# Kernel tuning notes

Measured on AMD Instinct MI355X. Metric: run time of the kernel, lower is better.

Reference implementation:

```python
import jax, jax.numpy as jnp
import numpy as np

B, L, D_MODEL, D_STATE, D_CONV, EXPAND = 2, 1024, 1024, 16, 4, 2
D_INNER = D_MODEL * EXPAND


def setup_inputs() -> dict:
    key = jax.random.key(0)
    ks = jax.random.split(key, 8)
    s = lambda fan: 1.0 / np.sqrt(fan)
    x = jax.random.normal(ks[0], (B, L, D_MODEL), jnp.float32)
    in_proj_w = jax.random.normal(ks[1], (D_MODEL, 2 * D_INNER), jnp.float32) * s(D_MODEL)
    conv_w = jax.random.normal(ks[2], (D_INNER, 1, D_CONV), jnp.float32) * s(D_CONV)
    conv_b = jax.random.normal(ks[3], (D_INNER,), jnp.float32) * 0.01
    x_proj_w = jax.random.normal(ks[4], (D_INNER, 2 * D_STATE + D_INNER), jnp.float32) * s(D_INNER)
    dt_proj_w = jax.random.normal(ks[5], (D_INNER, D_INNER), jnp.float32) * s(D_INNER)
    dt_proj_b = jax.random.normal(ks[6], (D_INNER,), jnp.float32) * 0.01
    A_log = jnp.log(jnp.tile(jnp.arange(1, D_STATE + 1, dtype=jnp.float32)[None, :], (D_INNER, 1)))
    D = jnp.ones((D_INNER,), jnp.float32)
    out_proj_w = jax.random.normal(ks[7], (D_INNER, D_MODEL), jnp.float32) * s(D_INNER)
    return {"x": x, "in_proj_w": in_proj_w, "conv_w": conv_w, "conv_b": conv_b,
            "x_proj_w": x_proj_w, "dt_proj_w": dt_proj_w, "dt_proj_b": dt_proj_b,
            "A_log": A_log, "D": D, "out_proj_w": out_proj_w}


def _mamba_forward(x, in_proj_w, conv_w, conv_b, x_proj_w, dt_proj_w, dt_proj_b, A_log, D, out_proj_w):
    Bb, Ll, _ = x.shape
    d_inner, _, d_conv = conv_w.shape
    d_state = A_log.shape[1]
    # input projection and gate split
    xz = x @ in_proj_w                       # [B, L, 2*Di]
    x_inner, z = jnp.split(xz, 2, axis=-1)   # each [B, L, Di]
    # causal depthwise conv (left pad k-1, truncate to L == torch pad+slice)
    xc = jnp.transpose(x_inner, (0, 2, 1))   # [B, Di, L]
    xc = jax.lax.conv_general_dilated(
        xc, conv_w, window_strides=(1,), padding=[(d_conv - 1, 0)],
        dimension_numbers=("NCH", "OIH", "NCH"), feature_group_count=d_inner)
    xc = xc + conv_b[None, :, None]
    u = jax.nn.silu(jnp.transpose(xc, (0, 2, 1)))  # [B, L, Di]
    # SSM parameter projections
    ssm = u @ x_proj_w                        # [B, L, 2N+Di]
    B_ssm = ssm[..., :d_state]                # [B, L, N]
    C_ssm = ssm[..., d_state:2 * d_state]     # [B, L, N]
    dt = jax.nn.softplus(ssm[..., 2 * d_state:] @ dt_proj_w + dt_proj_b)  # [B, L, Di]
    A_real = -jnp.exp(A_log)                  # [Di, N]
    # selective scan over sequence (recurrence via lax.scan)
    def step(h, inp):
        dt_t, B_t, u_t = inp                  # [B,Di], [B,N], [B,Di]
        dA = jnp.exp(dt_t[..., None] * A_real)            # [B, Di, N]
        dBu = dt_t[..., None] * B_t[:, None, :] * u_t[..., None]
        h = dA * h + dBu
        return h, h
    h0 = jnp.zeros((Bb, d_inner, d_state), x.dtype)
    xs = (jnp.swapaxes(dt, 0, 1), jnp.swapaxes(B_ssm, 0, 1), jnp.swapaxes(u, 0, 1))
    _, states = jax.lax.scan(step, h0, xs)    # [L, B, Di, N]
    y = jnp.einsum("lbdn,lbn->lbd", states, jnp.swapaxes(C_ssm, 0, 1))
    y = jnp.swapaxes(y, 0, 1) + D * u         # skip connection
    y = y * jax.nn.silu(z)                    # gating
    return y @ out_proj_w                     # [B, L, d_model]


def reference(x, in_proj_w, conv_w, conv_b, x_proj_w, dt_proj_w, dt_proj_b, A_log, D, out_proj_w):
    return _mamba_forward(x, in_proj_w, conv_w, conv_b, x_proj_w, dt_proj_w, dt_proj_b, A_log, D, out_proj_w)
```

## Files before the change

kernel.cpp:

```cpp
#include <hip/hip_runtime.h>
#include <hip/hip_bf16.h>

#define BB 2
#define LL 1024
#define DMODEL 1024
#define DINNER 2048
#define DSTATE 16
#define DCONV 4
#define MM (BB * LL)
#define N_XZ 4096
#define N_SSM 2080
#define N_SSM_PAD 2176
#define CCH 32
#define LCH 32

typedef __hip_bfloat16 bf16;
typedef short bf16x8 __attribute__((ext_vector_type(8)));
typedef float f32x4 __attribute__((ext_vector_type(4)));

__device__ __forceinline__ void load16_lds(const bf16* g, bf16* l) {
    __builtin_amdgcn_global_load_lds(
        (const __attribute__((address_space(1))) void*)g,
        (__attribute__((address_space(3))) void*)l,
        16, 0, 0);
}

__global__ void cvt_kernel(const float* __restrict__ in, bf16* __restrict__ out, int n) {
    int i = blockIdx.x * blockDim.x + threadIdx.x;
    if (i < n) out[i] = __float2bfloat16(in[i]);
}

__global__ void transpose_cvt_kernel(const float* __restrict__ in, bf16* __restrict__ out,
                                     int K, int N) {
    __shared__ float tile[32][33];
    const int nb = blockIdx.x * 32, kb = blockIdx.y * 32;
    const int tx = threadIdx.x & 31;
    const int ty = threadIdx.x >> 5;
    #pragma unroll
    for (int i = 0; i < 32; i += 8) {
        int k = kb + ty + i, n = nb + tx;
        tile[ty + i][tx] = (k < K && n < N) ? in[(size_t)k * N + n] : 0.f;
    }
    __syncthreads();
    #pragma unroll
    for (int i = 0; i < 32; i += 8) {
        int n = nb + ty + i, k = kb + tx;
        if (n < N && k < K) out[(size_t)n * K + k] = __float2bfloat16(tile[tx][ty + i]);
    }
}

#define TM 128
#define TN 64
#define TK 32
template<int EPI, int KSPLIT = 1>
__global__ __launch_bounds__(256) void mfma_gemm(
    const bf16* __restrict__ A, int lda,
    const bf16* __restrict__ Wt, int ldw,
    float* __restrict__ Cf, bf16* __restrict__ Cb, int ldc,
    const float* __restrict__ bias,
    int N, int K)
{
    __shared__ __align__(16) bf16 As[TM * TK];
    __shared__ __align__(16) bf16 Bs[TN * TK];
    const int tid = threadIdx.x;
    const int wave = tid >> 6, lane = tid & 63;
    const int wm = (wave >> 1) * 64, wn = (wave & 1) * 32;
    const int m0 = blockIdx.y * TM, n0 = blockIdx.x * TN;
    const int lm = lane & 15, kq = lane >> 4;

    const int srow = lane >> 2;
    const int cg = ((lane & 3) - ((srow >> 1) & 3)) & 3;
    const bf16* gA0 = A + (size_t)(m0 + wave * 16 + srow) * lda + cg * 8;
    const bf16* gA1 = A + (size_t)(m0 + wave * 16 + 64 + srow) * lda + cg * 8;
    const bf16* gB  = Wt + (size_t)(n0 + wave * 16 + srow) * ldw + cg * 8;
    bf16* As0 = &As[(wave * 16) * TK];
    bf16* As1 = &As[(wave * 16 + 64) * TK];
    bf16* Bs0 = &Bs[(wave * 16) * TK];

    const int soff = ((kq + ((lm >> 1) & 3)) & 3) * 8;

    const int Kc = K / KSPLIT;
    const int kbeg = (KSPLIT > 1) ? blockIdx.z * Kc : 0;

    f32x4 acc[4][2] = {};

    for (int it = 0; it < Kc; it += TK) {
        const int k0 = kbeg + it;
        load16_lds(gA0 + k0, As0);
        load16_lds(gA1 + k0, As1);
        load16_lds(gB + k0, Bs0);
        __syncthreads();

        bf16x8 af[4], bfr[2];
        #pragma unroll
        for (int i = 0; i < 4; ++i)
            af[i] = *(const bf16x8*)(&As[(wm + i * 16 + lm) * TK + soff]);
        #pragma unroll
        for (int j = 0; j < 2; ++j)
            bfr[j] = *(const bf16x8*)(&Bs[(wn + j * 16 + lm) * TK + soff]);
        #pragma unroll
        for (int i = 0; i < 4; ++i)
            #pragma unroll
            for (int j = 0; j < 2; ++j)
                acc[i][j] = __builtin_amdgcn_mfma_f32_16x16x32_bf16(af[i], bfr[j], acc[i][j], 0, 0, 0);
        __syncthreads();
    }

    #pragma unroll
    for (int i = 0; i < 4; ++i) {
        #pragma unroll
        for (int j = 0; j < 2; ++j) {
            int gcol = n0 + wn + j * 16 + lm;
            if ((EPI == 0 || EPI == 3) && gcol >= N) continue;
            #pragma unroll
            for (int r = 0; r < 4; ++r) {
                int grow = m0 + wm + i * 16 + kq * 4 + r;
                float v = acc[i][j][r];
                if (EPI == 1) {
                    v += bias[gcol];
                    v = (v > 20.f) ? v : log1pf(__expf(v));
                    Cf[(size_t)grow * ldc + gcol] = v;
                } else if (EPI == 2) {
                    if (KSPLIT > 1) atomicAdd(&Cf[(size_t)grow * ldc + gcol], v);
                    else            Cf[(size_t)grow * ldc + gcol] = v;
                } else if (EPI == 3) {
                    if (gcol < 32) Cf[(size_t)grow * 32 + gcol] = v;
                    else           Cb[(size_t)grow * ldc + gcol] = __float2bfloat16(v);
                } else {
                    Cb[(size_t)grow * ldc + gcol] = __float2bfloat16(v);
                }
            }
        }
    }
}

__global__ void conv_silu_kernel(const bf16* __restrict__ xz,
                                 const float* __restrict__ conv_w,
                                 const float* __restrict__ conv_b,
                                 bf16* __restrict__ u)
{
    int idx = blockIdx.x * blockDim.x + threadIdx.x;
    if (idx >= BB * LL * DINNER) return;
    int d = idx & (DINNER - 1);
    int l = (idx >> 11) & (LL - 1);
    int b = idx >> 21;
    float acc = conv_b[d];
    #pragma unroll
    for (int j = 0; j < DCONV; ++j) {
        int ll = l - (DCONV - 1) + j;
        if (ll >= 0) {
            float xv = (float)xz[((size_t)(b * LL + ll)) * N_XZ + d];
            acc = fmaf(conv_w[d * DCONV + j], xv, acc);
        }
    }
    u[idx] = __float2bfloat16(acc / (1.f + __expf(-acc)));
}

__global__ __launch_bounds__(256) void scan_phase_a(
    const float* __restrict__ dt, const bf16* __restrict__ u,
    const float* __restrict__ BC,
    const float* __restrict__ A_log,
    float* __restrict__ chunkP, float* __restrict__ chunkH)
{
    const int d = blockIdx.x * 256 + threadIdx.x;
    const int c = blockIdx.y, b = blockIdx.z;
    const int l0 = c * LCH;

    float A[DSTATE];
    {
        const f32x4* ap = (const f32x4*)(A_log + d * DSTATE);
        #pragma unroll
        for (int q = 0; q < 4; ++q) {
            f32x4 v = ap[q];
            #pragma unroll
            for (int r = 0; r < 4; ++r) A[q * 4 + r] = -__expf(v[r]);
        }
    }
    float h[DSTATE];
    #pragma unroll
    for (int n = 0; n < DSTATE; ++n) h[n] = 0.f;
    float sdt = 0.f;

    const float* dtp = dt + ((size_t)b * LL + l0) * DINNER + d;
    const bf16* up = u + ((size_t)b * LL + l0) * DINNER + d;
    const float* bcp = BC + ((size_t)b * LL + l0) * 32;

    #pragma unroll 2
    for (int i = 0; i < LCH; ++i) {
        float dtv = *dtp;
        float uv  = (float)*up;
        float du  = dtv * uv;
        f32x4 Bv[4];
        #pragma unroll
        for (int q = 0; q < 4; ++q) Bv[q] = *(const f32x4*)(bcp + q * 4);
        #pragma unroll
        for (int n = 0; n < DSTATE; ++n) {
            float a = __expf(dtv * A[n]);
            h[n] = fmaf(a, h[n], du * Bv[n >> 2][n & 3]);
        }
        sdt += dtv;
        dtp += DINNER; up += DINNER; bcp += 32;
    }

    size_t idx = (((size_t)b * CCH + c) * DINNER + d) * DSTATE;
    #pragma unroll
    for (int q = 0; q < 4; ++q) {
        f32x4 pv, hv;
        #pragma unroll
        for (int r = 0; r < 4; ++r) { pv[r] = __expf(A[q * 4 + r] * sdt); hv[r] = h[q * 4 + r]; }
        *(f32x4*)(chunkP + idx + q * 4) = pv;
        *(f32x4*)(chunkH + idx + q * 4) = hv;
    }
}

__global__ __launch_bounds__(256) void scan_phase_p(
    const float* __restrict__ chunkP, float* __restrict__ chunkH)
{
    int gid = blockIdx.x * 256 + threadIdx.x;
    int n = gid & 15;
    int d = (gid >> 4) & (DINNER - 1);
    int b = gid >> 15;
    const size_t stride = (size_t)DINNER * DSTATE;
    size_t idx = ((size_t)b * CCH * DINNER + d) * DSTATE + n;
    float H = 0.f;
    for (int c = 0; c < CCH; ++c) {
        float P  = chunkP[idx];
        float hl = chunkH[idx];
        chunkH[idx] = H;
        H = fmaf(P, H, hl);
        idx += stride;
    }
}

__global__ __launch_bounds__(256) void scan_phase_b(
    const float* __restrict__ dt, bf16* __restrict__ u,
    const float* __restrict__ BC, const bf16* __restrict__ xz,
    const float* __restrict__ A_log, const float* __restrict__ Dp,
    const float* __restrict__ chunkH)
{
    const int d = blockIdx.x * 256 + threadIdx.x;
    const int c = blockIdx.y, b = blockIdx.z;
    const int l0 = c * LCH;

    float A[DSTATE];
    {
        const f32x4* ap = (const f32x4*)(A_log + d * DSTATE);
        #pragma unroll
        for (int q = 0; q < 4; ++q) {
            f32x4 v = ap[q];
            #pragma unroll
            for (int r = 0; r < 4; ++r) A[q * 4 + r] = -__expf(v[r]);
        }
    }
    const float Dd = Dp[d];
    float h[DSTATE];
    {
        size_t idx = (((size_t)b * CCH + c) * DINNER + d) * DSTATE;
        #pragma unroll
        for (int q = 0; q < 4; ++q) {
            f32x4 v = *(const f32x4*)(chunkH + idx + q * 4);
            #pragma unroll
            for (int r = 0; r < 4; ++r) h[q * 4 + r] = v[r];
        }
    }

    const float* dtp = dt + ((size_t)b * LL + l0) * DINNER + d;
    bf16* up = u + ((size_t)b * LL + l0) * DINNER + d;
    const float* bcp = BC + ((size_t)b * LL + l0) * 32;
    const bf16* zp = xz + ((size_t)b * LL + l0) * N_XZ + DINNER + d;

    #pragma unroll 2
    for (int i = 0; i < LCH; ++i) {
        float dtv = *dtp;
        float uv  = (float)*up;
        float du  = dtv * uv;
        f32x4 Bv[4], Cv[4];
        #pragma unroll
        for (int q = 0; q < 4; ++q) {
            Bv[q] = *(const f32x4*)(bcp + q * 4);
            Cv[q] = *(const f32x4*)(bcp + 16 + q * 4);
        }
        float acc = 0.f;
        #pragma unroll
        for (int n = 0; n < DSTATE; ++n) {
            float a = __expf(dtv * A[n]);
            h[n] = fmaf(a, h[n], du * Bv[n >> 2][n & 3]);
            acc = fmaf(h[n], Cv[n >> 2][n & 3], acc);
        }
        float zv = (float)*zp;
        acc = fmaf(Dd, uv, acc);
        acc *= zv / (1.f + __expf(-zv));
        *up = __float2bfloat16(acc);
        dtp += DINNER; up += DINNER; bcp += 32; zp += N_XZ;
    }
}

extern "C" void kernel_launch(void* const* d_in, const int* in_sizes, int n_in,
                              void* d_out, int out_size, void* d_ws, size_t ws_size,
                              hipStream_t stream) {
    const float* x         = (const float*)d_in[0];
    const float* in_proj_w = (const float*)d_in[1];
    const float* conv_w    = (const float*)d_in[2];
    const float* conv_b    = (const float*)d_in[3];
    const float* x_proj_w  = (const float*)d_in[4];
    const float* dt_proj_w = (const float*)d_in[5];
    const float* dt_proj_b = (const float*)d_in[6];
    const float* A_log     = (const float*)d_in[7];
    const float* Dp        = (const float*)d_in[8];
    const float* out_proj_w= (const float*)d_in[9];
    float* out = (float*)d_out;

    char* p = (char*)d_ws;
    float* dt   = (float*)p;                          p += (size_t)MM * DINNER * 4;
    bf16*  xbf  = (bf16*)dt;
    bf16*  xz   = (bf16*)p;                           p += (size_t)MM * N_XZ * 2;
    bf16*  u    = (bf16*)p;                           p += (size_t)MM * DINNER * 2;
    bf16*  ssm  = (bf16*)p;                           p += (size_t)MM * N_SSM * 2;
    bf16*  Wt1  = (bf16*)p;                           p += (size_t)N_XZ * DMODEL * 2;
    bf16*  Wt2  = (bf16*)p;                           p += (size_t)N_SSM_PAD * DINNER * 2;
    bf16*  Wt3  = (bf16*)p;                           p += (size_t)DINNER * DINNER * 2;
    bf16*  Wt4  = (bf16*)p;                           p += (size_t)DMODEL * DINNER * 2;
    float* BC   = (float*)p;                          p += (size_t)MM * 32 * 4;
    float* chunkP = (float*)Wt1;
    float* chunkH = (float*)Wt2;

    {
        int n = MM * DMODEL;
        cvt_kernel<<<(n + 255) / 256, 256, 0, stream>>>(x, xbf, n);
        transpose_cvt_kernel<<<dim3(N_XZ / 32, DMODEL / 32), 256, 0, stream>>>(in_proj_w, Wt1, DMODEL, N_XZ);
        transpose_cvt_kernel<<<dim3((N_SSM + 31) / 32, DINNER / 32), 256, 0, stream>>>(x_proj_w, Wt2, DINNER, N_SSM);
        transpose_cvt_kernel<<<dim3(DINNER / 32, DINNER / 32), 256, 0, stream>>>(dt_proj_w, Wt3, DINNER, DINNER);
        transpose_cvt_kernel<<<dim3(DMODEL / 32, DINNER / 32), 256, 0, stream>>>(out_proj_w, Wt4, DINNER, DMODEL);
    }
    mfma_gemm<0><<<dim3(N_XZ / TN, MM / TM), 256, 0, stream>>>(
        xbf, DMODEL, Wt1, DMODEL, nullptr, xz, N_XZ, nullptr, N_XZ, DMODEL);
    {
        int n = BB * LL * DINNER;
        conv_silu_kernel<<<(n + 255) / 256, 256, 0, stream>>>(xz, conv_w, conv_b, u);
    }
    mfma_gemm<3><<<dim3(N_SSM_PAD / TN, MM / TM), 256, 0, stream>>>(
        u, DINNER, Wt2, DINNER, BC, ssm, N_SSM, nullptr, N_SSM, DINNER);
    mfma_gemm<1><<<dim3(DINNER / TN, MM / TM), 256, 0, stream>>>(
        ssm + 2 * DSTATE, N_SSM, Wt3, DINNER, dt, nullptr, DINNER, dt_proj_b, DINNER, DINNER);
    scan_phase_a<<<dim3(DINNER / 256, CCH, BB), 256, 0, stream>>>(dt, u, BC, A_log, chunkP, chunkH);
    scan_phase_p<<<dim3(BB * DINNER * DSTATE / 256), 256, 0, stream>>>(chunkP, chunkH);
    scan_phase_b<<<dim3(DINNER / 256, CCH, BB), 256, 0, stream>>>(dt, u, BC, xz, A_log, Dp, chunkH);
    hipMemsetAsync(out, 0, (size_t)out_size * sizeof(float), stream);
    mfma_gemm<2, 2><<<dim3(DMODEL / TN, MM / TM, 2), 256, 0, stream>>>(
        u, DINNER, Wt4, DINNER, out, nullptr, DMODEL, nullptr, DMODEL, DINNER);
}
```

Before: 374.7 us.

## Fuse weight/input conversion launches and double GEMM K-tile with XOR swizzle

Merges the five float-to-bf16 conversion and transpose launches into a single prep kernel that dispatches on block index. It also vectorizes the x conversion with float4 loads. The GEMM K-tile grows from 32 to 64, with a new XOR-swizzled LDS layout and two MFMA k-steps per barrier pair, so the loop synchronizes half as often. The cost is larger LDS tiles and more fragment registers per thread, which may lower occupancy.

```diff
diff --git a/kernel.cpp b/kernel.cpp
--- a/kernel.cpp
+++ b/kernel.cpp
@@ -25,33 +25,48 @@
         16, 0, 0);
 }
 
-__global__ void cvt_kernel(const float* __restrict__ in, bf16* __restrict__ out, int n) {
-    int i = blockIdx.x * blockDim.x + threadIdx.x;
-    if (i < n) out[i] = __float2bfloat16(in[i]);
-}
-
-__global__ void transpose_cvt_kernel(const float* __restrict__ in, bf16* __restrict__ out,
-                                     int K, int N) {
+__global__ __launch_bounds__(256) void prep_kernel(
+    const float* __restrict__ x, bf16* __restrict__ xbf,
+    const float* __restrict__ w1, bf16* __restrict__ o1,
+    const float* __restrict__ w2, bf16* __restrict__ o2,
+    const float* __restrict__ w3, bf16* __restrict__ o3,
+    const float* __restrict__ w4, bf16* __restrict__ o4)
+{
+    int bid = blockIdx.x;
+    const float* src; bf16* dst; int K, N, tn, tk;
+    if (bid < 4096)        { src = w1; dst = o1; K = 1024; N = 4096; tn = bid & 127; tk = bid >> 7; }
+    else if (bid < 8256)   { bid -= 4096;  src = w2; dst = o2; K = 2048; N = 2080; tn = bid % 65; tk = bid / 65; }
+    else if (bid < 12352)  { bid -= 8256;  src = w3; dst = o3; K = 2048; N = 2048; tn = bid & 63; tk = bid >> 6; }
+    else if (bid < 14400)  { bid -= 12352; src = w4; dst = o4; K = 2048; N = 1024; tn = bid & 31; tk = bid >> 5; }
+    else {
+        bid -= 14400;
+        int i = (bid * 256 + threadIdx.x) * 4;
+        float4 v = *(const float4*)(x + i);
+        xbf[i + 0] = __float2bfloat16(v.x);
+        xbf[i + 1] = __float2bfloat16(v.y);
+        xbf[i + 2] = __float2bfloat16(v.z);
+        xbf[i + 3] = __float2bfloat16(v.w);
+        return;
+    }
     __shared__ float tile[32][33];
-    const int nb = blockIdx.x * 32, kb = blockIdx.y * 32;
-    const int tx = threadIdx.x & 31;
-    const int ty = threadIdx.x >> 5;
+    const int nb = tn * 32, kb = tk * 32;
+    const int tx = threadIdx.x & 31, ty = threadIdx.x >> 5;
     #pragma unroll
     for (int i = 0; i < 32; i += 8) {
         int k = kb + ty + i, n = nb + tx;
-        tile[ty + i][tx] = (k < K && n < N) ? in[(size_t)k * N + n] : 0.f;
+        tile[ty + i][tx] = (k < K && n < N) ? src[(size_t)k * N + n] : 0.f;
     }
     __syncthreads();
     #pragma unroll
     for (int i = 0; i < 32; i += 8) {
         int n = nb + ty + i, k = kb + tx;
-        if (n < N && k < K) out[(size_t)n * K + k] = __float2bfloat16(tile[tx][ty + i]);
+        if (n < N && k < K) dst[(size_t)n * K + k] = __float2bfloat16(tile[tx][ty + i]);
     }
 }
 
 #define TM 128
 #define TN 64
-#define TK 32
+#define TK 64
 template<int EPI, int KSPLIT = 1>
 __global__ __launch_bounds__(256) void mfma_gemm(
     const bf16* __restrict__ A, int lda,
@@ -68,41 +83,47 @@
     const int m0 = blockIdx.y * TM, n0 = blockIdx.x * TN;
     const int lm = lane & 15, kq = lane >> 4;
 
-    const int srow = lane >> 2;
-    const int cg = ((lane & 3) - ((srow >> 1) & 3)) & 3;
-    const bf16* gA0 = A + (size_t)(m0 + wave * 16 + srow) * lda + cg * 8;
-    const bf16* gA1 = A + (size_t)(m0 + wave * 16 + 64 + srow) * lda + cg * 8;
-    const bf16* gB  = Wt + (size_t)(n0 + wave * 16 + srow) * ldw + cg * 8;
-    bf16* As0 = &As[(wave * 16) * TK];
-    bf16* As1 = &As[(wave * 16 + 64) * TK];
-    bf16* Bs0 = &Bs[(wave * 16) * TK];
-
-    const int soff = ((kq + ((lm >> 1) & 3)) & 3) * 8;
+    const int srow = lane >> 3;
+    const int schunk = (lane & 7) ^ srow;
+    const bf16* gA = A + (size_t)(m0 + wave * 32 + srow) * lda + schunk * 8;
+    const bf16* gB = Wt + (size_t)(n0 + wave * 16 + srow) * ldw + schunk * 8;
+    bf16* lA = &As[(wave * 32) * TK];
+    bf16* lB = &Bs[(wave * 16) * TK];
 
     const int Kc = K / KSPLIT;
     const int kbeg = (KSPLIT > 1) ? blockIdx.z * Kc : 0;
 
     f32x4 acc[4][2] = {};
+    const int fsw = (lm & 7);
 
     for (int it = 0; it < Kc; it += TK) {
         const int k0 = kbeg + it;
-        load16_lds(gA0 + k0, As0);
-        load16_lds(gA1 + k0, As1);
-        load16_lds(gB + k0, Bs0);
+        #pragma unroll
+        for (int g = 0; g < 4; ++g)
+            load16_lds(gA + (size_t)(8 * g) * lda + k0, lA + (8 * g) * TK);
+        #pragma unroll
+        for (int g = 0; g < 2; ++g)
+            load16_lds(gB + (size_t)(8 * g) * ldw + k0, lB + (8 * g) * TK);
         __syncthreads();
 
-        bf16x8 af[4], bfr[2];
+        bf16x8 af[4][2], bfr[2][2];
         #pragma unroll
         for (int i = 0; i < 4; ++i)
-            af[i] = *(const bf16x8*)(&As[(wm + i * 16 + lm) * TK + soff]);
+            #pragma unroll
+            for (int t = 0; t < 2; ++t)
+                af[i][t] = *(const bf16x8*)(&As[(wm + i * 16 + lm) * TK + ((t * 4 + kq) ^ fsw) * 8]);
         #pragma unroll
         for (int j = 0; j < 2; ++j)
-            bfr[j] = *(const bf16x8*)(&Bs[(wn + j * 16 + lm) * TK + soff]);
-        #pragma unroll
-        for (int i = 0; i < 4; ++i)
-            #pragma unroll
-            for (int j = 0; j < 2; ++j)
-                acc[i][j] = __builtin_amdgcn_mfma_f32_16x16x32_bf16(af[i], bfr[j], acc[i][j], 0, 0, 0);
+            #pragma unroll
+            for (int t = 0; t < 2; ++t)
+                bfr[j][t] = *(const bf16x8*)(&Bs[(wn + j * 16 + lm) * TK + ((t * 4 + kq) ^ fsw) * 8]);
+        #pragma unroll
+        for (int t = 0; t < 2; ++t)
+            #pragma unroll
+            for (int i = 0; i < 4; ++i)
+                #pragma unroll
+                for (int j = 0; j < 2; ++j)
+                    acc[i][j] = __builtin_amdgcn_mfma_f32_16x16x32_bf16(af[i][t], bfr[j][t], acc[i][j], 0, 0, 0);
         __syncthreads();
     }
 
@@ -324,14 +345,8 @@
     float* chunkP = (float*)Wt1;
     float* chunkH = (float*)Wt2;
 
-    {
-        int n = MM * DMODEL;
-        cvt_kernel<<<(n + 255) / 256, 256, 0, stream>>>(x, xbf, n);
-        transpose_cvt_kernel<<<dim3(N_XZ / 32, DMODEL / 32), 256, 0, stream>>>(in_proj_w, Wt1, DMODEL, N_XZ);
-        transpose_cvt_kernel<<<dim3((N_SSM + 31) / 32, DINNER / 32), 256, 0, stream>>>(x_proj_w, Wt2, DINNER, N_SSM);
-        transpose_cvt_kernel<<<dim3(DINNER / 32, DINNER / 32), 256, 0, stream>>>(dt_proj_w, Wt3, DINNER, DINNER);
-        transpose_cvt_kernel<<<dim3(DMODEL / 32, DINNER / 32), 256, 0, stream>>>(out_proj_w, Wt4, DINNER, DMODEL);
-    }
+    prep_kernel<<<16448, 256, 0, stream>>>(x, xbf, in_proj_w, Wt1, x_proj_w, Wt2,
+                                           dt_proj_w, Wt3, out_proj_w, Wt4);
     mfma_gemm<0><<<dim3(N_XZ / TN, MM / TM), 256, 0, stream>>>(
         xbf, DMODEL, Wt1, DMODEL, nullptr, xz, N_XZ, nullptr, N_XZ, DMODEL);
     {
```

Result: faster. 340.0 us (-9.3%).
